# Kernel tuning notes

Measured on AMD Instinct MI355X. Metric: run time of the kernel, lower is better.

Reference implementation:

```python
import jax, jax.numpy as jnp
import numpy as np

D_MODEL = 1024
N_HEADS = 16
HEAD_DIM = D_MODEL // N_HEADS


def setup_inputs() -> dict:
    key = jax.random.key(0)
    kx, kq, kk, kv, ko = jax.random.split(key, 5)
    B, T = 4, 2048
    s = 1.0 / np.sqrt(D_MODEL)
    return {
        "x": jax.random.normal(kx, (B, T, D_MODEL), dtype=jnp.float32),
        "W_Q": jax.random.normal(kq, (D_MODEL, D_MODEL), dtype=jnp.float32) * s,
        "W_K": jax.random.normal(kk, (D_MODEL, D_MODEL), dtype=jnp.float32) * s,
        "W_V": jax.random.normal(kv, (D_MODEL, D_MODEL), dtype=jnp.float32) * s,
        "W_O": jax.random.normal(ko, (D_MODEL, D_MODEL), dtype=jnp.float32) * s,
    }


def reference(x, W_Q, W_K, W_V, W_O):
    B, T, C = x.shape
    H, hd = N_HEADS, HEAD_DIM
    # nn.Linear applies x @ W.T; W_* here are the [out,in] weight matrices.
    def proj(W):
        return (x @ W.T).reshape(B, T, H, hd).transpose(0, 2, 1, 3)  # [B,H,T,hd]
    q, k, v = proj(W_Q), proj(W_K), proj(W_V)
    scale = 1.0 / np.sqrt(hd).astype(np.float32)
    attn = jnp.einsum("bhqd,bhkd->bhqk", q, k) * scale  # [B,H,T,T]
    causal = jnp.tril(jnp.ones((T, T), dtype=bool))
    attn = jnp.where(causal, attn, -jnp.inf)
    attn = jax.nn.softmax(attn, axis=-1)
    out = jnp.einsum("bhqk,bhkd->bhqd", attn, v)  # [B,H,T,hd]
    out = out.transpose(0, 2, 1, 3).reshape(B, T, C)
    return out @ W_O.T
```

## Files before the change

### kernel.cpp

```cpp
#include <hip/hip_runtime.h>
#include <hip/hip_bf16.h>
#include <stdint.h>


typedef __attribute__((ext_vector_type(8))) short short8;
typedef __attribute__((ext_vector_type(4))) short short4v;
typedef __attribute__((ext_vector_type(4))) float floatx4;

#define LOG2E 1.4426950408889634f

__device__ __forceinline__ void gload_lds16(const void* g, void* l) {
  __builtin_amdgcn_global_load_lds(
      (const __attribute__((address_space(1))) void*)g,
      (__attribute__((address_space(3))) void*)l, 16, 0, 0);
}

__device__ __forceinline__ short f2bf(float f) {
  __hip_bfloat16 h = __float2bfloat16(f);
  return *reinterpret_cast<short*>(&h);
}

__global__ __launch_bounds__(256) void cvt_f32_bf16(const float* __restrict__ src,
                                                    short* __restrict__ dst, int n4,
                                                    float scale) {
  const int i = blockIdx.x * blockDim.x + threadIdx.x;
  if (i >= n4) return;
  const float4 v = reinterpret_cast<const float4*>(src)[i];
  short4v o;
  o.x = f2bf(v.x * scale); o.y = f2bf(v.y * scale);
  o.z = f2bf(v.z * scale); o.w = f2bf(v.w * scale);
  reinterpret_cast<short4v*>(dst)[i] = o;
}

__global__ __launch_bounds__(256) void cvt_weights(const float* __restrict__ wq,
                                                   const float* __restrict__ wk,
                                                   const float* __restrict__ wv,
                                                   const float* __restrict__ wo,
                                                   short* __restrict__ dst0,
                                                   float qscale) {
  const int y = blockIdx.y;
  const float* src = (y == 0) ? wq : (y == 1) ? wk : (y == 2) ? wv : wo;
  const float scale = (y == 0) ? qscale : 1.0f;
  short* dst = dst0 + (size_t)y * 1048576;
  const int i = blockIdx.x * blockDim.x + threadIdx.x;
  const float4 v = reinterpret_cast<const float4*>(src)[i];
  short4v o;
  o.x = f2bf(v.x * scale); o.y = f2bf(v.y * scale);
  o.z = f2bf(v.z * scale); o.w = f2bf(v.w * scale);
  reinterpret_cast<short4v*>(&dst[i * 4])[0] = o;
}

template <int MODE>
__device__ __forceinline__ void gemm256_body(const short* __restrict__ A,
                                             const short* __restrict__ B,
                                             void* __restrict__ Cout,
                                             int m0, int n0,
                                             short* __restrict__ la0,
                                             short* __restrict__ la1,
                                             short* __restrict__ lb0,
                                             short* __restrict__ lb1) {
  const int tid = threadIdx.x;
  const int lane = tid & 63;
  const int w = tid >> 6;
  const int wm = w >> 1, wn = w & 1;
  const int lrow = lane & 15, lgrp = lane >> 4;

  floatx4 acc[4][4] = {};

  const int srow = tid >> 3;
  const int scb = (tid & 7) ^ (srow & 7);
  const short* ag = A + (size_t)(m0 + srow) * 1024 + scb * 8;
  const short* bg = B + (size_t)(n0 + srow) * 1024 + scb * 8;

  auto stage_a3 = [&](short* la) {
    gload_lds16(ag, la + tid * 8);
    gload_lds16(ag + 64 * 1024, la + (512 + tid) * 8);
    gload_lds16(ag + 128 * 1024, la + (1024 + tid) * 8);
  };
  auto stage_b3 = [&](short* la, short* lb) {
    gload_lds16(ag + 192 * 1024, la + (1536 + tid) * 8);
    gload_lds16(bg, lb + tid * 8);
    gload_lds16(bg + 64 * 1024, lb + (512 + tid) * 8);
  };

  short8 af[2][4];
  auto loadA = [&](const short* la) {
#pragma unroll
    for (int mf = 0; mf < 4; ++mf) {
      const int row = wm * 64 + mf * 16 + lrow;
#pragma unroll
      for (int kk = 0; kk < 2; ++kk)
        af[kk][mf] = *reinterpret_cast<const short8*>(
            &la[row * 64 + (((kk * 4 + lgrp) ^ (row & 7)) * 8)]);
    }
  };
  auto half = [&](const short* lb, int nh) {
    short8 bf[2][2];
#pragma unroll
    for (int nf = 0; nf < 2; ++nf) {
      const int row = wn * 64 + (nh * 2 + nf) * 16 + lrow;
#pragma unroll
      for (int kk = 0; kk < 2; ++kk)
        bf[kk][nf] = *reinterpret_cast<const short8*>(
            &lb[row * 64 + (((kk * 4 + lgrp) ^ (row & 7)) * 8)]);
    }
    __builtin_amdgcn_s_setprio(1);
#pragma unroll
    for (int kk = 0; kk < 2; ++kk)
#pragma unroll
      for (int mf = 0; mf < 4; ++mf)
#pragma unroll
        for (int nf = 0; nf < 2; ++nf)
          acc[mf][nh * 2 + nf] = __builtin_amdgcn_mfma_f32_16x16x32_bf16(
              af[kk][mf], bf[kk][nf], acc[mf][nh * 2 + nf], 0, 0, 0);
    __builtin_amdgcn_s_setprio(0);
  };

  auto iter_pre = [&](const short* lac, const short* lbc, short* lan, short* lbn) {
    stage_a3(lan);
    asm volatile("s_waitcnt vmcnt(3)" ::: "memory");
    __builtin_amdgcn_s_barrier();
    __builtin_amdgcn_sched_barrier(0);
    loadA(lac);
    half(lbc, 0);
    stage_b3(lan, lbn);
    ag += 64; bg += 64;
    half(lbc, 1);
    __builtin_amdgcn_sched_barrier(0);
    __builtin_amdgcn_s_barrier();
    __builtin_amdgcn_sched_barrier(0);
  };

  stage_a3(la0);
  stage_b3(la0, lb0);
  ag += 64; bg += 64;

#pragma unroll 1
  for (int kt = 0; kt < 12; kt += 2) {
    iter_pre(la0, lb0, la1, lb1);
    iter_pre(la1, lb1, la0, lb0);
  }
  iter_pre(la0, lb0, la1, lb1);
  iter_pre(la1, lb1, la0, lb0);
  iter_pre(la0, lb0, la1, lb1);
  {
    asm volatile("s_waitcnt vmcnt(0)" ::: "memory");
    __builtin_amdgcn_s_barrier();
    __builtin_amdgcn_sched_barrier(0);
    loadA(la1);
    half(lb1, 0);
    half(lb1, 1);
  }

#pragma unroll
  for (int mf = 0; mf < 4; ++mf) {
#pragma unroll
    for (int nf = 0; nf < 4; ++nf) {
      if (MODE == 2) {
        short4v pk;
#pragma unroll
        for (int r = 0; r < 4; ++r) pk[r] = f2bf(acc[mf][nf][r]);
        const int t0 = m0 + wm * 64 + mf * 16 + lgrp * 4;
        const int ch = n0 + wn * 64 + nf * 16 + lrow;
        const int bh = ((t0 >> 11) << 4) + (ch >> 6);
        short* Vt = reinterpret_cast<short*>(Cout);
        *reinterpret_cast<short4v*>(
            &Vt[(size_t)bh * 131072 + (size_t)(ch & 63) * 2048 + (t0 & 2047)]) = pk;
      } else {
#pragma unroll
        for (int r = 0; r < 4; ++r) {
          const int grow = m0 + wm * 64 + mf * 16 + lgrp * 4 + r;
          const int gcol = n0 + wn * 64 + nf * 16 + lrow;
          if (MODE == 1)
            reinterpret_cast<short*>(Cout)[(size_t)grow * 1024 + gcol] = f2bf(acc[mf][nf][r]);
          else
            reinterpret_cast<float*>(Cout)[(size_t)grow * 1024 + gcol] = acc[mf][nf][r];
        }
      }
    }
  }
}

__global__ __launch_bounds__(512) void gemm_qkv(
    const short* __restrict__ xb, const short* __restrict__ wq, const short* __restrict__ wk,
    const short* __restrict__ wv, short* __restrict__ Qb, short* __restrict__ Kb,
    short* __restrict__ Vt) {
  __shared__ short lds_a[2][256 * 64];
  __shared__ short lds_b[2][128 * 64];
  const int flat = blockIdx.x;
  const int xcd = flat & 7, rest = flat >> 3;
  const int nblk = rest & 7, pg = rest >> 3;
  const int panel = pg * 8 + xcd;
  const int m = panel & 31, z = panel >> 5;
  const int m0 = m * 256, n0 = nblk * 128;
  if (z == 0)
    gemm256_body<1>(xb, wq, Qb, m0, n0, lds_a[0], lds_a[1], lds_b[0], lds_b[1]);
  else if (z == 1)
    gemm256_body<1>(xb, wk, Kb, m0, n0, lds_a[0], lds_a[1], lds_b[0], lds_b[1]);
  else
    gemm256_body<2>(xb, wv, Vt, m0, n0, lds_a[0], lds_a[1], lds_b[0], lds_b[1]);
}

__global__ __launch_bounds__(512) void gemm_out(const short* __restrict__ Ob,
                                                const short* __restrict__ wo,
                                                float* __restrict__ out) {
  __shared__ short lds_a[2][256 * 64];
  __shared__ short lds_b[2][128 * 64];
  const int flat = blockIdx.x;
  const int xcd = flat & 7, rest = flat >> 3;
  const int nblk = rest & 7, pg = rest >> 3;
  const int panel = pg * 8 + xcd;
  gemm256_body<0>(Ob, wo, out, panel * 256, nblk * 128,
                  lds_a[0], lds_a[1], lds_b[0], lds_b[1]);
}

__global__ __launch_bounds__(256, 4) void attn_fwd(const short* __restrict__ Q,
                                                   const short* __restrict__ K,
                                                   const short* __restrict__ Vt,
                                                   short* __restrict__ O) {
  __shared__ short lds_k[2][64 * 64];
  __shared__ short lds_v[2][64 * 64];
  __shared__ short lds_p[4][16 * 64];

  const int tid = threadIdx.x;
  const int lane = tid & 63;
  const int w = tid >> 6;
  const int lrow = lane & 15, lgrp = lane >> 4;
  const int flat = blockIdx.x;
  const int bh = flat & 63;
  const int p = flat >> 6;
  const int b = bh >> 4, h = bh & 15;

  const size_t base = (size_t)b * 2048 * 1024 + h * 64;
  const size_t vbase = (size_t)bh * 131072;

  const int srow = tid >> 3;
  const int scb = (tid & 7) ^ (srow & 7);
  const size_t koff = (size_t)srow * 1024 + scb * 8;
  const size_t voff = (size_t)srow * 2048 + scb * 8;
  short* const kd0 = &lds_k[0][tid * 8];
  short* const kd1 = &lds_k[1][tid * 8];
  short* const vd0 = &lds_v[0][tid * 8];
  short* const vd1 = &lds_v[1][tid * 8];

  auto stageK = [&](short* ldst, const short* gsrc) {
    gload_lds16(gsrc, ldst);
    gload_lds16(gsrc + 32 * 1024, ldst + 2048);
  };
  auto stageV = [&](short* ldst, const short* gsrc) {
    gload_lds16(gsrc, ldst);
    gload_lds16(gsrc + 32 * 2048, ldst + 2048);
  };

#pragma unroll 1
  for (int pass = 0; pass < 2; ++pass) {
    const int qc = pass == 0 ? (31 - p) : p;
    const int qw = qc * 64 + w * 16;
    const int nkb = qc + 1;

    short8 qf0, qf1;
    {
      const short* qp = Q + base + (size_t)(qw + lrow) * 1024 + lgrp * 8;
      qf0 = *reinterpret_cast<const short8*>(qp);
      qf1 = *reinterpret_cast<const short8*>(qp + 32);
    }

    floatx4 oacc[4] = {};
    float lsum = 0.f;

    const short* kg = K + base + koff;
    const short* vg = Vt + vbase + voff;

    auto body = [&](int kb, const short* __restrict__ ldsk,
                    const short* __restrict__ ldsv) {
      floatx4 s[4];
      __builtin_amdgcn_s_setprio(1);
#pragma unroll
      for (int nf = 0; nf < 4; ++nf) {
        const short8 kf0 = *reinterpret_cast<const short8*>(
            &ldsk[(nf * 16 + lrow) * 64 + ((lgrp) ^ (lrow & 7)) * 8]);
        const short8 kf1 = *reinterpret_cast<const short8*>(
            &ldsk[(nf * 16 + lrow) * 64 + ((4 + lgrp) ^ (lrow & 7)) * 8]);
        floatx4 z = {};
        z = __builtin_amdgcn_mfma_f32_16x16x32_bf16(kf0, qf0, z, 0, 0, 0);
        z = __builtin_amdgcn_mfma_f32_16x16x32_bf16(kf1, qf1, z, 0, 0, 0);
        s[nf] = z;
      }
      __builtin_amdgcn_s_setprio(0);

      if (kb == qc) {
#pragma unroll
        for (int nf = 0; nf < 4; ++nf)
#pragma unroll
          for (int r = 0; r < 4; ++r)
            if (nf * 16 + lgrp * 4 + r > w * 16 + lrow) s[nf][r] = -1e30f;
      }

#pragma unroll
      for (int nf = 0; nf < 4; ++nf) {
        const float p0 = __builtin_amdgcn_exp2f(s[nf][0]);
        const float p1 = __builtin_amdgcn_exp2f(s[nf][1]);
        const float p2 = __builtin_amdgcn_exp2f(s[nf][2]);
        const float p3 = __builtin_amdgcn_exp2f(s[nf][3]);
        lsum += (p0 + p1) + (p2 + p3);
        short4v pk;
        pk.x = f2bf(p0); pk.y = f2bf(p1); pk.z = f2bf(p2); pk.w = f2bf(p3);
        const int c8 = (nf * 4 + lgrp) ^ ((lrow & 7) << 1);
        *reinterpret_cast<short4v*>(&lds_p[w][lrow * 64 + c8 * 4]) = pk;
      }

      short8 pa0, pa1;
      {
        const int c0 = (lgrp) ^ (lrow & 7);
        const int c1 = (4 + lgrp) ^ (lrow & 7);
        pa0 = *reinterpret_cast<const short8*>(&lds_p[w][lrow * 64 + c0 * 8]);
        pa1 = *reinterpret_cast<const short8*>(&lds_p[w][lrow * 64 + c1 * 8]);
      }
      __builtin_amdgcn_s_setprio(1);
#pragma unroll
      for (int nf = 0; nf < 4; ++nf) {
        const short8 vf0 = *reinterpret_cast<const short8*>(
            &ldsv[(nf * 16 + lrow) * 64 + ((lgrp) ^ (lrow & 7)) * 8]);
        const short8 vf1 = *reinterpret_cast<const short8*>(
            &ldsv[(nf * 16 + lrow) * 64 + ((4 + lgrp) ^ (lrow & 7)) * 8]);
        oacc[nf] = __builtin_amdgcn_mfma_f32_16x16x32_bf16(pa0, vf0, oacc[nf], 0, 0, 0);
        oacc[nf] = __builtin_amdgcn_mfma_f32_16x16x32_bf16(pa1, vf1, oacc[nf], 0, 0, 0);
      }
      __builtin_amdgcn_s_setprio(0);
    };

    stageK(kd0, kg); kg += 65536;
    stageV(vd0, vg); vg += 64;
    __syncthreads();

#pragma unroll 1
    for (int kb = 0; kb < nkb; kb += 2) {
      if (kb + 1 < nkb) { stageK(kd1, kg); kg += 65536; stageV(vd1, vg); vg += 64; }
      body(kb, lds_k[0], lds_v[0]);
      __syncthreads();
      if (kb + 1 >= nkb) break;
      if (kb + 2 < nkb) { stageK(kd0, kg); kg += 65536; stageV(vd0, vg); vg += 64; }
      body(kb + 1, lds_k[1], lds_v[1]);
      __syncthreads();
    }

    lsum += __shfl_xor(lsum, 16, 64);
    lsum += __shfl_xor(lsum, 32, 64);
#pragma unroll
    for (int r = 0; r < 4; ++r) {
      const float linv = 1.0f / __shfl(lsum, lgrp * 4 + r, 64);
      const int t = qw + lgrp * 4 + r;
#pragma unroll
      for (int nf = 0; nf < 4; ++nf)
        O[base + (size_t)t * 1024 + nf * 16 + lrow] = f2bf(oacc[nf][r] * linv);
    }
  }
}

extern "C" void kernel_launch(void* const* d_in, const int* in_sizes, int n_in,
                              void* d_out, int out_size, void* d_ws, size_t ws_size,
                              hipStream_t stream) {
  const float* x  = (const float*)d_in[0];
  const float* Wq = (const float*)d_in[1];
  const float* Wk = (const float*)d_in[2];
  const float* Wv = (const float*)d_in[3];
  const float* Wo = (const float*)d_in[4];

  uint8_t* ws = (uint8_t*)d_ws;
  short* xb  = (short*)(ws + 0);
  short* wqb = (short*)(ws + 16777216);
  short* wkb = (short*)(ws + 18874368);
  short* wvb = (short*)(ws + 20971520);
  short* wob = (short*)(ws + 23068672);
  short* Qb  = (short*)(ws + 25165824);
  short* Kb  = (short*)(ws + 41943040);
  short* Vt  = (short*)(ws + 58720256);
  short* Ob  = (short*)(ws + 75497472);
  if (ws_size < 92274688ull) return;

  const float qscale = 0.125f * LOG2E;

  cvt_f32_bf16<<<8192, 256, 0, stream>>>(x, xb, 2097152, 1.0f);
  cvt_weights<<<dim3(1024, 4), 256, 0, stream>>>(Wq, Wk, Wv, Wo, wqb, qscale);

  gemm_qkv<<<768, 512, 0, stream>>>(xb, wqb, wkb, wvb, Qb, Kb, Vt);
  attn_fwd<<<1024, 256, 0, stream>>>(Qb, Kb, Vt, Ob);
  gemm_out<<<256, 512, 0, stream>>>(Ob, wob, (float*)d_out);
}
```

Before: 156.3 us.

## Triple-buffer GEMM LDS tiles with a prefetch distance of two

The shared GEMM body moves from a double-buffered LDS pipeline with split A/B staging and two barriers per k-step to a three-buffer ring. Each step now has a single barrier and issues all six async global-to-LDS loads for the tile two steps ahead before computing the current one. The aim is to hide more global-load latency and cut synchronisation in both the QKV and output projections. In exchange, LDS use rises to about 144KB per block, which leaves less headroom.

After: 159.2 us. About the same (+1.8%).

```diff
diff --git a/kernel.cpp b/kernel.cpp
--- a/kernel.cpp
+++ b/kernel.cpp
@@ -57,8 +57,10 @@
                                              int m0, int n0,
                                              short* __restrict__ la0,
                                              short* __restrict__ la1,
+                                             short* __restrict__ la2,
                                              short* __restrict__ lb0,
-                                             short* __restrict__ lb1) {
+                                             short* __restrict__ lb1,
+                                             short* __restrict__ lb2) {
   const int tid = threadIdx.x;
   const int lane = tid & 63;
   const int w = tid >> 6;
@@ -72,15 +74,14 @@
   const short* ag = A + (size_t)(m0 + srow) * 1024 + scb * 8;
   const short* bg = B + (size_t)(n0 + srow) * 1024 + scb * 8;
 
-  auto stage_a3 = [&](short* la) {
+  auto stage6 = [&](short* la, short* lb) {
     gload_lds16(ag, la + tid * 8);
     gload_lds16(ag + 64 * 1024, la + (512 + tid) * 8);
     gload_lds16(ag + 128 * 1024, la + (1024 + tid) * 8);
-  };
-  auto stage_b3 = [&](short* la, short* lb) {
     gload_lds16(ag + 192 * 1024, la + (1536 + tid) * 8);
     gload_lds16(bg, lb + tid * 8);
     gload_lds16(bg + 64 * 1024, lb + (512 + tid) * 8);
+    ag += 64; bg += 64;
   };
 
   short8 af[2][4];
@@ -115,41 +116,44 @@
               af[kk][mf], bf[kk][nf], acc[mf][nh * 2 + nf], 0, 0, 0);
     __builtin_amdgcn_s_setprio(0);
   };
-
-  auto iter_pre = [&](const short* lac, const short* lbc, short* lan, short* lbn) {
-    stage_a3(lan);
-    asm volatile("s_waitcnt vmcnt(3)" ::: "memory");
+  auto compute = [&](const short* la, const short* lb) {
+    loadA(la);
+    half(lb, 0);
+    half(lb, 1);
+  };
+  auto iter_main = [&](const short* ca, const short* cb, short* na, short* nb) {
+    __builtin_amdgcn_sched_barrier(0);
+    asm volatile("s_waitcnt vmcnt(6)" ::: "memory");
     __builtin_amdgcn_s_barrier();
     __builtin_amdgcn_sched_barrier(0);
-    loadA(lac);
-    half(lbc, 0);
-    stage_b3(lan, lbn);
-    ag += 64; bg += 64;
-    half(lbc, 1);
-    __builtin_amdgcn_sched_barrier(0);
+    stage6(na, nb);
+    compute(ca, cb);
+  };
+
+  stage6(la0, lb0);
+  stage6(la1, lb1);
+
+#pragma unroll 1
+  for (int kt = 0; kt < 12; kt += 3) {
+    iter_main(la0, lb0, la2, lb2);
+    iter_main(la1, lb1, la0, lb0);
+    iter_main(la2, lb2, la1, lb1);
+  }
+  iter_main(la0, lb0, la2, lb2);
+  iter_main(la1, lb1, la0, lb0);
+  {
+    __builtin_amdgcn_sched_barrier(0);
+    asm volatile("s_waitcnt vmcnt(6)" ::: "memory");
     __builtin_amdgcn_s_barrier();
     __builtin_amdgcn_sched_barrier(0);
-  };
-
-  stage_a3(la0);
-  stage_b3(la0, lb0);
-  ag += 64; bg += 64;
-
-#pragma unroll 1
-  for (int kt = 0; kt < 12; kt += 2) {
-    iter_pre(la0, lb0, la1, lb1);
-    iter_pre(la1, lb1, la0, lb0);
-  }
-  iter_pre(la0, lb0, la1, lb1);
-  iter_pre(la1, lb1, la0, lb0);
-  iter_pre(la0, lb0, la1, lb1);
+    compute(la2, lb2);
+  }
   {
+    __builtin_amdgcn_sched_barrier(0);
     asm volatile("s_waitcnt vmcnt(0)" ::: "memory");
     __builtin_amdgcn_s_barrier();
     __builtin_amdgcn_sched_barrier(0);
-    loadA(la1);
-    half(lb1, 0);
-    half(lb1, 1);
+    compute(la0, lb0);
   }
 
 #pragma unroll
@@ -185,8 +189,8 @@
     const short* __restrict__ xb, const short* __restrict__ wq, const short* __restrict__ wk,
     const short* __restrict__ wv, short* __restrict__ Qb, short* __restrict__ Kb,
     short* __restrict__ Vt) {
-  __shared__ short lds_a[2][256 * 64];
-  __shared__ short lds_b[2][128 * 64];
+  __shared__ short lds_a[3][256 * 64];
+  __shared__ short lds_b[3][128 * 64];
   const int flat = blockIdx.x;
   const int xcd = flat & 7, rest = flat >> 3;
   const int nblk = rest & 7, pg = rest >> 3;
@@ -194,24 +198,27 @@
   const int m = panel & 31, z = panel >> 5;
   const int m0 = m * 256, n0 = nblk * 128;
   if (z == 0)
-    gemm256_body<1>(xb, wq, Qb, m0, n0, lds_a[0], lds_a[1], lds_b[0], lds_b[1]);
+    gemm256_body<1>(xb, wq, Qb, m0, n0, lds_a[0], lds_a[1], lds_a[2],
+                    lds_b[0], lds_b[1], lds_b[2]);
   else if (z == 1)
-    gemm256_body<1>(xb, wk, Kb, m0, n0, lds_a[0], lds_a[1], lds_b[0], lds_b[1]);
+    gemm256_body<1>(xb, wk, Kb, m0, n0, lds_a[0], lds_a[1], lds_a[2],
+                    lds_b[0], lds_b[1], lds_b[2]);
   else
-    gemm256_body<2>(xb, wv, Vt, m0, n0, lds_a[0], lds_a[1], lds_b[0], lds_b[1]);
+    gemm256_body<2>(xb, wv, Vt, m0, n0, lds_a[0], lds_a[1], lds_a[2],
+                    lds_b[0], lds_b[1], lds_b[2]);
 }
 
 __global__ __launch_bounds__(512) void gemm_out(const short* __restrict__ Ob,
                                                 const short* __restrict__ wo,
                                                 float* __restrict__ out) {
-  __shared__ short lds_a[2][256 * 64];
-  __shared__ short lds_b[2][128 * 64];
+  __shared__ short lds_a[3][256 * 64];
+  __shared__ short lds_b[3][128 * 64];
   const int flat = blockIdx.x;
   const int xcd = flat & 7, rest = flat >> 3;
   const int nblk = rest & 7, pg = rest >> 3;
   const int panel = pg * 8 + xcd;
   gemm256_body<0>(Ob, wo, out, panel * 256, nblk * 128,
-                  lds_a[0], lds_a[1], lds_b[0], lds_b[1]);
+                  lds_a[0], lds_a[1], lds_a[2], lds_b[0], lds_b[1], lds_b[2]);
 }
 
 __global__ __launch_bounds__(256, 4) void attn_fwd(const short* __restrict__ Q,
```
